# Performance work log

Hardware: AMD Instinct MI355X
Metric: run time of the kernel (lower is better)

Reference implementation:

```python
import jax, jax.numpy as jnp
import numpy as np

N = 8192; S = 32; M = 8; H = 64; DIM = 3
DELTA_T = 0.1; WELL_WIDTH = 1.0; WELL_DEPTH = 1.0
LN_EPS = 1e-5; FOUR_PI = 4.0 * np.pi


def _mlp(x, W1, b1, g, h, W2, b2):
    # eqx: Linear -> LayerNorm -> relu -> Linear, vmapped over cells
    y = x @ W1.T + b1
    mu = y.mean(-1, keepdims=True)
    var = y.var(-1, keepdims=True)
    y = g * (y - mu) / jnp.sqrt(var + LN_EPS) + h
    return jax.nn.relu(y) @ W2.T + b2


def setup_inputs():
    key = jax.random.key(0)
    ks = jax.random.split(key, 16)
    w = lambda k, shape, s=0.05: jax.random.normal(k, shape, jnp.float32) * s
    return {
        "position": jax.random.normal(ks[0], (N, DIM), jnp.float32) * 10.0,
        "radius": jax.random.uniform(ks[1], (N,), jnp.float32, 0.5, 1.5),
        "state": jax.random.uniform(ks[2], (N, S), jnp.float32),
        "diffusion_coefs": jax.random.uniform(ks[3], (M,), jnp.float32, 0.5, 2.0),
        "degradation_rates": jax.random.uniform(ks[4], (M,), jnp.float32, 0.1, 1.0),
        "Wsec1": w(ks[5], (H, S)), "bsec1": jnp.zeros((H,)), "gsec": jnp.ones((H,)), "hsec": jnp.zeros((H,)),
        "Wsec2": w(ks[6], (M, H)), "bsec2": jnp.zeros((M,)),
        "Wsen1": w(ks[7], (H, S + M)), "bsen1": jnp.zeros((H,)), "gsen": jnp.ones((H,)), "hsen": jnp.zeros((H,)),
        "Wsen2": w(ks[8], (S, H)), "bsen2": jnp.zeros((S,)),
        "Wr1": w(ks[9], (H, S)), "br1": jnp.zeros((H,)), "gr": jnp.ones((H,)), "hr": jnp.zeros((H,)),
        "Wr2": w(ks[10], (S, H)), "br2": jnp.zeros((S,)),
        "Wm1": w(ks[11], (H, S)), "bm1": jnp.zeros((H,)), "gm": jnp.ones((H,)), "hm": jnp.zeros((H,)),
        "Wm2": w(ks[12], (DIM, H)), "bm2": jnp.zeros((DIM,)),
        "active": jnp.ones((N,), bool),
    }


def _forward(position, radius, state, diffusion_coefs, degradation_rates,
             Wsec1, bsec1, gsec, hsec, Wsec2, bsec2,
             Wsen1, bsen1, gsen, hsen, Wsen2, bsen2,
             Wr1, br1, gr, hr, Wr2, br2,
             Wm1, bm1, gm, hm, Wm2, bm2,
             active):
    act = active.astype(position.dtype)
    # pairwise distances (N, N) without materializing (N, N, 3)
    sq = jnp.sum(position * position, axis=-1)
    d2 = sq[:, None] + sq[None, :] - 2.0 * (position @ position.T)
    d = jnp.sqrt(jnp.clip(d2, 1e-12))
    # --- SecretionModel: relu MLP over state ---
    secretion = jax.nn.relu(_mlp(state, Wsec1, bsec1, gsec, hsec, Wsec2, bsec2)) * act[:, None]
    # --- DiffusionModel: steady-state Green's fn exp(-r/lambda) / (4 pi D r) ---
    d_eff = jnp.maximum(d, radius[None, :])  # regularize at/inside source cell
    conc = []
    for m in range(M):  # small fixed loop over molecules
        Dm = jnp.clip(diffusion_coefs[m], 1e-3)
        km = jnp.clip(degradation_rates[m], 1e-3)
        lam = jnp.sqrt(Dm / km)
        K = jnp.exp(-d_eff / lam) / (FOUR_PI * Dm * d_eff)  # (N, N)
        conc.append(K @ secretion[:, m])
    concentration = jnp.stack(conc, axis=-1) * act[:, None]  # (N, M)
    # --- SensationModel: state += MLP([state, concentration]) ---
    state = state + _mlp(jnp.concatenate([state, concentration], axis=-1),
                         Wsen1, bsen1, gsen, hsen, Wsen2, bsen2)
    # --- ReactModel: state += sigmoid(MLP(state)) ---
    state = state + jax.nn.sigmoid(_mlp(state, Wr1, br1, gr, hr, Wr2, br2))
    # --- MotilityModel: per-cell force ---
    motility = _mlp(state, Wm1, bm1, gm, hm, Wm2, bm2)  # (N, DIM)
    # --- MechanicsModel: pairwise Morse force, F_i = sum_j f(d_ij) (p_i - p_j)/d_ij ---
    a = 1.0 / WELL_WIDTH
    re = radius[:, None] + radius[None, :]
    e = jnp.exp(-a * (d - re))
    fmag = 2.0 * a * WELL_DEPTH * (e * e - e)  # = -dU/dd, repulsive for d < re
    mask = act[:, None] * act[None, :] * (1.0 - jnp.eye(d.shape[0], dtype=d.dtype))
    coef = fmag * mask / d  # (N, N)
    mech = position * coef.sum(axis=1, keepdims=True) - coef @ position  # avoids (N,N,3)
    # --- integrate positions ---
    force = (mech + motility) * act[:, None]
    position = position + DELTA_T * force
    return jnp.concatenate([position, state, concentration], axis=-1)  # (N, DIM+S+M)


def reference(position, radius, state, diffusion_coefs, degradation_rates,
              Wsec1, bsec1, gsec, hsec, Wsec2, bsec2,
              Wsen1, bsen1, gsen, hsen, Wsen2, bsen2,
              Wr1, br1, gr, hr, Wr2, br2,
              Wm1, bm1, gm, hm, Wm2, bm2,
              active):
    return _forward(position, radius, state, diffusion_coefs, degradation_rates,
                    Wsec1, bsec1, gsec, hsec, Wsec2, bsec2,
                    Wsen1, bsen1, gsen, hsen, Wsen2, bsen2,
                    Wr1, br1, gr, hr, Wr2, br2,
                    Wm1, bm1, gm, hm, Wm2, bm2,
                    active)
```

## Files before the change

kernel.cpp:

```cpp
#include <hip/hip_runtime.h>
#include <math.h>

#define N_CELLS 8192
#define S_DIM   32
#define M_MOL   8
#define H_DIM   64
#define LN_EPS  1e-5f
#define FOUR_PI 12.566370614359172f
#define LOG2E   1.4426950408889634f
#define DT      0.1f

#define TI      4

#define REC_F    16
#define PART_OFF (N_CELLS * REC_F)
#define PART_F   12
#define WS_NEED(NJC) ((size_t)(PART_OFF + (size_t)N_CELLS * (NJC) * PART_F) * 4)

typedef float v2f __attribute__((ext_vector_type(2)));

__device__ __forceinline__ v2f vfma2(v2f a, v2f b, v2f c) {
#if __has_builtin(__builtin_elementwise_fma)
    return __builtin_elementwise_fma(a, b, c);
#else
    v2f r; r.x = fmaf(a.x, b.x, c.x); r.y = fmaf(a.y, b.y, c.y); return r;
#endif
}
__device__ __forceinline__ v2f vmax2(v2f a, v2f b) {
#if __has_builtin(__builtin_elementwise_max)
    return __builtin_elementwise_max(a, b);
#else
    v2f r; r.x = fmaxf(a.x, b.x); r.y = fmaxf(a.y, b.y); return r;
#endif
}
__device__ __forceinline__ v2f vmin2(v2f a, v2f b) {
#if __has_builtin(__builtin_elementwise_min)
    return __builtin_elementwise_min(a, b);
#else
    v2f r; r.x = fminf(a.x, b.x); r.y = fminf(a.y, b.y); return r;
#endif
}

__device__ __forceinline__ float fast_exp2(float x) {
#if __has_builtin(__builtin_amdgcn_exp2f)
    return __builtin_amdgcn_exp2f(x);
#else
    return exp2f(x);
#endif
}
__device__ __forceinline__ float fast_rcp(float x) {
#if __has_builtin(__builtin_amdgcn_rcpf)
    return __builtin_amdgcn_rcpf(x);
#else
    return 1.0f / x;
#endif
}
__device__ __forceinline__ float fast_rsqrt(float x) {
#if __has_builtin(__builtin_amdgcn_rsqf)
    return __builtin_amdgcn_rsqf(x);
#else
    return rsqrtf(x);
#endif
}
__device__ __forceinline__ float fast_log2(float x) {
#if __has_builtin(__builtin_amdgcn_logf)
    return __builtin_amdgcn_logf(x);
#else
    return log2f(x);
#endif
}

__device__ __forceinline__ float wave_sum(float v) {
#pragma unroll
    for (int off = 32; off > 0; off >>= 1) v += __shfl_xor(v, off, 64);
    return v;
}

__device__ __forceinline__ float ln_relu(float y, const float* __restrict__ g,
                                         const float* __restrict__ hh, int lane) {
    float mu  = wave_sum(y) * (1.0f / 64.0f);
    float t   = y - mu;
    float var = wave_sum(t * t) * (1.0f / 64.0f);
    float r   = fmaf(g[lane], t * fast_rsqrt(var + LN_EPS), hh[lane]);
    return fmaxf(r, 0.0f);
}

__global__ __launch_bounds__(256) void k_secretion(
    const float* __restrict__ pos, const float* __restrict__ radius,
    const float* __restrict__ state, const float* __restrict__ dc,
    const float* __restrict__ dr,
    const float* __restrict__ W1, const float* __restrict__ b1,
    const float* __restrict__ g,  const float* __restrict__ hh,
    const float* __restrict__ W2, const float* __restrict__ b2,
    float* __restrict__ ws)
{
    __shared__ float W1t[S_DIM * H_DIM];
    __shared__ float W2o[M_MOL * H_DIM];

    int tid = threadIdx.x;
    for (int idx = tid; idx < S_DIM * H_DIM; idx += 256) {
        int h = idx / S_DIM, k = idx % S_DIM;
        W1t[k * H_DIM + h] = W1[idx];
    }
    for (int idx = tid; idx < M_MOL * H_DIM; idx += 256) W2o[idx] = W2[idx];

    float* acc = ws + PART_OFF;
    int gtid = blockIdx.x * 256 + tid;
    if (gtid < N_CELLS * PART_F) acc[gtid] = 0.0f;
    __syncthreads();

    int lane = tid & 63, wid = tid >> 6;
    int wave = blockIdx.x * 4 + wid;
#pragma unroll
    for (int c = 0; c < 2; ++c) {
        int cell = wave * 2 + c;
        float x = (lane < S_DIM) ? state[cell * S_DIM + lane] : 0.0f;
        float y = b1[lane];
#pragma unroll
        for (int k = 0; k < S_DIM; ++k)
            y = fmaf(W1t[k * H_DIM + lane], __shfl(x, k, 64), y);
        float yr = ln_relu(y, g, hh, lane);

        float sp[M_MOL];
#pragma unroll
        for (int m = 0; m < M_MOL; ++m) {
            float sm = wave_sum(W2o[m * H_DIM + lane] * yr) + b2[m];
            sm = fmaxf(sm, 0.0f);
            float Dm = fmaxf(dc[m], 1e-3f);
            sp[m] = fast_log2(fmaxf(sm / (FOUR_PI * Dm), 1e-38f));
        }
        float negc_slot = 0.0f;
        if (cell < M_MOL) {
            float Dm = fmaxf(dc[cell], 1e-3f);
            float km = fmaxf(dr[cell], 1e-3f);
            negc_slot = -LOG2E * sqrtf(km / Dm);
        }
        float px = pos[cell * 3 + 0], py = pos[cell * 3 + 1], pz = pos[cell * 3 + 2];
        float r = radius[cell];
        float invr = fast_rcp(r);
        float4 v;
        if (lane == 0)      v = make_float4(px, py, pz, r);
        else if (lane == 1) v = make_float4(invr, r * LOG2E, sp[0], sp[1]);
        else if (lane == 2) v = make_float4(sp[2], sp[3], sp[4], sp[5]);
        else                v = make_float4(sp[6], sp[7], negc_slot, 0.0f);
        if (lane < 4) ((float4*)ws)[cell * 4 + lane] = v;
    }
}

#define PAIR2(PX, PY, PZ, RIL, C0A, C0B, C0C, C0D, C1A, C1B, C1C, C1D, FX, FY, FZ) \
    {                                                                        \
        v2f dx = PX - pjx, dy = PY - pjy, dz = PZ - pjz;                     \
        v2f d2 = dx * dx; d2 = vfma2(dy, dy, d2); d2 = vfma2(dz, dz, d2);    \
        v2f epsv; epsv.x = 1e-12f; epsv.y = 1e-12f;                          \
        d2 = vmax2(d2, epsv);                                                \
        v2f rsq; rsq.x = fast_rsqrt(d2.x); rsq.y = fast_rsqrt(d2.y);         \
        v2f dd = d2 * rsq;                                                   \
        v2f arg = vfma2(dd, negL2, RIL + rlg);                               \
        v2f e; e.x = fast_exp2(arg.x); e.y = fast_exp2(arg.y);               \
        v2f q = vfma2(e, e, -e);                                             \
        v2f coef = q * rsq;                                                  \
        FX = vfma2(coef, dx, FX);                                            \
        FY = vfma2(coef, dy, FY);                                            \
        FZ = vfma2(coef, dz, FZ);                                            \
        v2f de = vmax2(dd, rj2);                                             \
        v2f iv = vmin2(rsq, ivr);                                            \
        {                                                                    \
            v2f de2; de2.x = de.x; de2.y = de.x;                             \
            v2f iv2; iv2.x = iv.x; iv2.y = iv.x;                             \
            v2f a0 = vfma2(de2, ng01, ls01);                                 \
            v2f a1 = vfma2(de2, ng23, ls23);                                 \
            v2f a2 = vfma2(de2, ng45, ls45);                                 \
            v2f a3 = vfma2(de2, ng67, ls67);                                 \
            v2f e0; e0.x = fast_exp2(a0.x); e0.y = fast_exp2(a0.y);          \
            v2f e1; e1.x = fast_exp2(a1.x); e1.y = fast_exp2(a1.y);          \
            v2f e2; e2.x = fast_exp2(a2.x); e2.y = fast_exp2(a2.y);          \
            v2f e3; e3.x = fast_exp2(a3.x); e3.y = fast_exp2(a3.y);          \
            C0A = vfma2(e0, iv2, C0A);                                       \
            C0B = vfma2(e1, iv2, C0B);                                       \
            C0C = vfma2(e2, iv2, C0C);                                       \
            C0D = vfma2(e3, iv2, C0D);                                       \
        }                                                                    \
        {                                                                    \
            v2f de2; de2.x = de.y; de2.y = de.y;                             \
            v2f iv2; iv2.x = iv.y; iv2.y = iv.y;                             \
            v2f a0 = vfma2(de2, ng01, ls01);                                 \
            v2f a1 = vfma2(de2, ng23, ls23);                                 \
            v2f a2 = vfma2(de2, ng45, ls45);                                 \
            v2f a3 = vfma2(de2, ng67, ls67);                                 \
            v2f e0; e0.x = fast_exp2(a0.x); e0.y = fast_exp2(a0.y);          \
            v2f e1; e1.x = fast_exp2(a1.x); e1.y = fast_exp2(a1.y);          \
            v2f e2; e2.x = fast_exp2(a2.x); e2.y = fast_exp2(a2.y);          \
            v2f e3; e3.x = fast_exp2(a3.x); e3.y = fast_exp2(a3.y);          \
            C1A = vfma2(e0, iv2, C1A);                                       \
            C1B = vfma2(e1, iv2, C1B);                                       \
            C1C = vfma2(e2, iv2, C1C);                                       \
            C1D = vfma2(e3, iv2, C1D);                                       \
        }                                                                    \
    }

template <int JC_T>
__global__ __launch_bounds__(256, 4) void k_pairwise(
    float* __restrict__ ws, int use_part)
{
    constexpr int NJC_T = N_CELLS / JC_T;
    __shared__ float4 Ls[JC_T * 4];
    int tid = threadIdx.x;
    int jbase = blockIdx.y * JC_T;
    const float4* rec4 = (const float4*)ws;
    for (int idx = tid; idx < JC_T * 4; idx += 256)
        Ls[idx] = rec4[jbase * 4 + idx];

    v2f ng01; ng01.x = ws[0 * REC_F + 14]; ng01.y = ws[1 * REC_F + 14];
    v2f ng23; ng23.x = ws[2 * REC_F + 14]; ng23.y = ws[3 * REC_F + 14];
    v2f ng45; ng45.x = ws[4 * REC_F + 14]; ng45.y = ws[5 * REC_F + 14];
    v2f ng67; ng67.x = ws[6 * REC_F + 14]; ng67.y = ws[7 * REC_F + 14];

    v2f negL2; negL2.x = -LOG2E; negL2.y = -LOG2E;

    int i0 = blockIdx.x * (256 * TI) + tid;
    float4 me0 = rec4[(size_t)(i0      ) * 4];
    float4 me1 = rec4[(size_t)(i0 + 256) * 4];
    float4 me2 = rec4[(size_t)(i0 + 512) * 4];
    float4 me3 = rec4[(size_t)(i0 + 768) * 4];
    v2f pxA; pxA.x = me0.x; pxA.y = me1.x;
    v2f pyA; pyA.x = me0.y; pyA.y = me1.y;
    v2f pzA; pzA.x = me0.z; pzA.y = me1.z;
    v2f riA; riA.x = me0.w * LOG2E; riA.y = me1.w * LOG2E;
    v2f pxB; pxB.x = me2.x; pxB.y = me3.x;
    v2f pyB; pyB.x = me2.y; pyB.y = me3.y;
    v2f pzB; pzB.x = me2.z; pzB.y = me3.z;
    v2f riB; riB.x = me2.w * LOG2E; riB.y = me3.w * LOG2E;

    v2f r0c0 = {0,0}, r0c1 = {0,0}, r0c2 = {0,0}, r0c3 = {0,0};
    v2f r1c0 = {0,0}, r1c1 = {0,0}, r1c2 = {0,0}, r1c3 = {0,0};
    v2f r2c0 = {0,0}, r2c1 = {0,0}, r2c2 = {0,0}, r2c3 = {0,0};
    v2f r3c0 = {0,0}, r3c1 = {0,0}, r3c2 = {0,0}, r3c3 = {0,0};
    v2f fAx = {0,0}, fAy = {0,0}, fAz = {0,0};
    v2f fBx = {0,0}, fBy = {0,0}, fBz = {0,0};
    __syncthreads();

#pragma unroll 2
    for (int jj = 0; jj < JC_T; ++jj) {
        float4 A  = Ls[jj * 4 + 0];
        float4 B  = Ls[jj * 4 + 1];
        float4 Cc = Ls[jj * 4 + 2];
        float4 Dd = Ls[jj * 4 + 3];
        v2f pjx; pjx.x = A.x; pjx.y = A.x;
        v2f pjy; pjy.x = A.y; pjy.y = A.y;
        v2f pjz; pjz.x = A.z; pjz.y = A.z;
        v2f rj2; rj2.x = A.w; rj2.y = A.w;
        v2f ivr; ivr.x = B.x; ivr.y = B.x;
        v2f rlg; rlg.x = B.y; rlg.y = B.y;
        v2f ls01; ls01.x = B.z;  ls01.y = B.w;
        v2f ls23; ls23.x = Cc.x; ls23.y = Cc.y;
        v2f ls45; ls45.x = Cc.z; ls45.y = Cc.w;
        v2f ls67; ls67.x = Dd.x; ls67.y = Dd.y;
        PAIR2(pxA, pyA, pzA, riA, r0c0, r0c1, r0c2, r0c3,
              r1c0, r1c1, r1c2, r1c3, fAx, fAy, fAz)
        PAIR2(pxB, pyB, pzB, riB, r2c0, r2c1, r2c2, r2c3,
              r3c0, r3c1, r3c2, r3c3, fBx, fBy, fBz)
    }

    if (use_part) {
#define STORE_ROW(IR, CA, CB, CCX, CD, FX, FY, FZ)                               \
        {                                                                        \
            float* p = ws + PART_OFF + (size_t)((IR) * NJC_T + blockIdx.y) * PART_F; \
            ((float4*)p)[0] = make_float4(CA.x, CA.y, CB.x, CB.y);               \
            ((float4*)p)[1] = make_float4(CCX.x, CCX.y, CD.x, CD.y);             \
            ((float4*)p)[2] = make_float4((FX) + (FX), (FY) + (FY), (FZ) + (FZ), 0.0f); \
        }
        STORE_ROW(i0,       r0c0, r0c1, r0c2, r0c3, fAx.x, fAy.x, fAz.x)
        STORE_ROW(i0 + 256, r1c0, r1c1, r1c2, r1c3, fAx.y, fAy.y, fAz.y)
        STORE_ROW(i0 + 512, r2c0, r2c1, r2c2, r2c3, fBx.x, fBy.x, fBz.x)
        STORE_ROW(i0 + 768, r3c0, r3c1, r3c2, r3c3, fBx.y, fBy.y, fBz.y)
#undef STORE_ROW
    } else {
#define ATOM_ROW(IR, CA, CB, CCX, CD, FX, FY, FZ)                                \
        {                                                                        \
            float* a = ws + PART_OFF + (size_t)(IR) * PART_F;                    \
            atomicAdd(&a[0], CA.x); atomicAdd(&a[1], CA.y);                      \
            atomicAdd(&a[2], CB.x); atomicAdd(&a[3], CB.y);                      \
            atomicAdd(&a[4], CCX.x); atomicAdd(&a[5], CCX.y);                    \
            atomicAdd(&a[6], CD.x); atomicAdd(&a[7], CD.y);                      \
            atomicAdd(&a[8], (FX) + (FX)); atomicAdd(&a[9], (FY) + (FY));        \
            atomicAdd(&a[10], (FZ) + (FZ));                                      \
        }
        ATOM_ROW(i0,       r0c0, r0c1, r0c2, r0c3, fAx.x, fAy.x, fAz.x)
        ATOM_ROW(i0 + 256, r1c0, r1c1, r1c2, r1c3, fAx.y, fAy.y, fAz.y)
        ATOM_ROW(i0 + 512, r2c0, r2c1, r2c2, r2c3, fBx.x, fBy.x, fBz.x)
        ATOM_ROW(i0 + 768, r3c0, r3c1, r3c2, r3c3, fBx.y, fBy.y, fBz.y)
#undef ATOM_ROW
    }
}

__global__ __launch_bounds__(256, 4) void k_update(
    const float* __restrict__ pos,   const float* __restrict__ state,
    const float* __restrict__ Wsen1, const float* __restrict__ bsen1,
    const float* __restrict__ gsen,  const float* __restrict__ hsen,
    const float* __restrict__ Wsen2, const float* __restrict__ bsen2,
    const float* __restrict__ Wr1,   const float* __restrict__ br1,
    const float* __restrict__ gr,    const float* __restrict__ hr,
    const float* __restrict__ Wr2,   const float* __restrict__ br2,
    const float* __restrict__ Wm1,   const float* __restrict__ bm1,
    const float* __restrict__ gm,    const float* __restrict__ hm,
    const float* __restrict__ Wm2,   const float* __restrict__ bm2,
    const float* __restrict__ ws,    float* __restrict__ out,
    int use_part, int njc)
{
    __shared__ float Ws1t[40 * 64];
    __shared__ float Ws2t[64 * 32];
    __shared__ float Wr1t[32 * 64];
    __shared__ float Wr2t[64 * 32];
    __shared__ float Wm1t[32 * 64];
    __shared__ float Wm2o[3 * 64];

    int tid = threadIdx.x;
    for (int idx = tid; idx < 40 * 64; idx += 256) { int h = idx / 40, k = idx % 40; Ws1t[k * 64 + h] = Wsen1[idx]; }
    for (int idx = tid; idx < 32 * 64; idx += 256) { int o = idx / 64, h = idx % 64; Ws2t[h * 32 + o] = Wsen2[idx]; }
    for (int idx = tid; idx < 32 * 64; idx += 256) { int h = idx / 32, k = idx % 32; Wr1t[k * 64 + h] = Wr1[idx]; }
    for (int idx = tid; idx < 32 * 64; idx += 256) { int o = idx / 64, h = idx % 64; Wr2t[h * 32 + o] = Wr2[idx]; }
    for (int idx = tid; idx < 32 * 64; idx += 256) { int h = idx / 32, k = idx % 32; Wm1t[k * 64 + h] = Wm1[idx]; }
    for (int idx = tid; idx < 3 * 64;  idx += 256) Wm2o[idx] = Wm2[idx];
    __syncthreads();

    int lane = tid & 63, wid = tid >> 6;
    int wave = blockIdx.x * 4 + wid;
    int o = lane & 31;
    int idx8 = lane & 7;

#pragma unroll
    for (int c = 0; c < 2; ++c) {
        int cell = wave * 2 + c;

        float r[12];
        if (use_part) {
#pragma unroll
            for (int m = 0; m < 12; ++m) r[m] = 0.0f;
            for (int s = lane; s < njc; s += 64) {
                const float* pb = ws + PART_OFF + (size_t)(cell * njc + s) * PART_F;
                float4 v0 = ((const float4*)pb)[0];
                float4 v1 = ((const float4*)pb)[1];
                float4 v2 = ((const float4*)pb)[2];
                r[0] += v0.x; r[1] += v0.y; r[2]  += v0.z; r[3]  += v0.w;
                r[4] += v1.x; r[5] += v1.y; r[6]  += v1.z; r[7]  += v1.w;
                r[8] += v2.x; r[9] += v2.y; r[10] += v2.z;
            }
#pragma unroll
            for (int m = 0; m < 11; ++m) r[m] = wave_sum(r[m]);
        } else {
            const float* ac = ws + PART_OFF + (size_t)cell * PART_F;
#pragma unroll
            for (int m = 0; m < 11; ++m) r[m] = ac[m];
        }
        float cv = r[0];
        cv = (idx8 == 1) ? r[1] : cv;
        cv = (idx8 == 2) ? r[2] : cv;
        cv = (idx8 == 3) ? r[3] : cv;
        cv = (idx8 == 4) ? r[4] : cv;
        cv = (idx8 == 5) ? r[5] : cv;
        cv = (idx8 == 6) ? r[6] : cv;
        cv = (idx8 == 7) ? r[7] : cv;

        float s_reg = (lane < 32) ? state[cell * 32 + lane] : 0.0f;

        float x = (lane < 32) ? s_reg : ((lane < 40) ? cv : 0.0f);
        float y = bsen1[lane];
#pragma unroll
        for (int k = 0; k < 40; ++k) y = fmaf(Ws1t[k * 64 + lane], __shfl(x, k, 64), y);
        float yr = ln_relu(y, gsen, hsen, lane);
        float a2 = 0.0f;
#pragma unroll
        for (int h = 0; h < 64; ++h) a2 = fmaf(Ws2t[h * 32 + o], __shfl(yr, h, 64), a2);
        s_reg += a2 + bsen2[o];

        y = br1[lane];
#pragma unroll
        for (int k = 0; k < 32; ++k) y = fmaf(Wr1t[k * 64 + lane], __shfl(s_reg, k, 64), y);
        yr = ln_relu(y, gr, hr, lane);
        a2 = 0.0f;
#pragma unroll
        for (int h = 0; h < 64; ++h) a2 = fmaf(Wr2t[h * 32 + o], __shfl(yr, h, 64), a2);
        a2 += br2[o];
        s_reg += fast_rcp(1.0f + fast_exp2(-a2 * LOG2E));

        y = bm1[lane];
#pragma unroll
        for (int k = 0; k < 32; ++k) y = fmaf(Wm1t[k * 64 + lane], __shfl(s_reg, k, 64), y);
        yr = ln_relu(y, gm, hm, lane);
        float mot[3];
#pragma unroll
        for (int m = 0; m < 3; ++m) mot[m] = wave_sum(Wm2o[m * 64 + lane] * yr) + bm2[m];

        float px = pos[cell * 3 + 0], py = pos[cell * 3 + 1], pz = pos[cell * 3 + 2];
        float nx = fmaf(DT, r[8] + mot[0], px);
        float ny = fmaf(DT, r[9] + mot[1], py);
        float nz = fmaf(DT, r[10] + mot[2], pz);

        float* orow = out + (size_t)cell * 43;
        float pv = (lane == 0) ? nx : ((lane == 1) ? ny : nz);
        if (lane < 3)  orow[lane] = pv;
        if (lane < 32) orow[3 + lane] = s_reg;
        if (lane < 8)  orow[35 + lane] = cv;
    }
}

extern "C" void kernel_launch(void* const* d_in, const int* in_sizes, int n_in,
                              void* d_out, int out_size, void* d_ws, size_t ws_size,
                              hipStream_t stream) {
    const float* pos    = (const float*)d_in[0];
    const float* radius = (const float*)d_in[1];
    const float* state  = (const float*)d_in[2];
    const float* dc     = (const float*)d_in[3];
    const float* dr     = (const float*)d_in[4];
    const float* Wsec1  = (const float*)d_in[5];
    const float* bsec1  = (const float*)d_in[6];
    const float* gsec   = (const float*)d_in[7];
    const float* hsec   = (const float*)d_in[8];
    const float* Wsec2  = (const float*)d_in[9];
    const float* bsec2  = (const float*)d_in[10];
    const float* Wsen1  = (const float*)d_in[11];
    const float* bsen1  = (const float*)d_in[12];
    const float* gsen   = (const float*)d_in[13];
    const float* hsen   = (const float*)d_in[14];
    const float* Wsen2  = (const float*)d_in[15];
    const float* bsen2  = (const float*)d_in[16];
    const float* Wr1    = (const float*)d_in[17];
    const float* br1    = (const float*)d_in[18];
    const float* gr     = (const float*)d_in[19];
    const float* hr     = (const float*)d_in[20];
    const float* Wr2    = (const float*)d_in[21];
    const float* br2    = (const float*)d_in[22];
    const float* Wm1    = (const float*)d_in[23];
    const float* bm1    = (const float*)d_in[24];
    const float* gm     = (const float*)d_in[25];
    const float* hm     = (const float*)d_in[26];
    const float* Wm2    = (const float*)d_in[27];
    const float* bm2    = (const float*)d_in[28];
    float* ws  = (float*)d_ws;
    float* out = (float*)d_out;

    int njc, use_part;
    if (ws_size >= WS_NEED(256))      { njc = 256; use_part = 1; }
    else if (ws_size >= WS_NEED(128)) { njc = 128; use_part = 1; }
    else if (ws_size >= WS_NEED(64))  { njc = 64;  use_part = 1; }
    else                              { njc = 64;  use_part = 0; }

    hipLaunchKernelGGL(k_secretion, dim3(1024), dim3(256), 0, stream,
                       pos, radius, state, dc, dr,
                       Wsec1, bsec1, gsec, hsec, Wsec2, bsec2, ws);
    if (njc == 256) {
        hipLaunchKernelGGL((k_pairwise<32>), dim3(N_CELLS / (256 * TI), 256), dim3(256), 0,
                           stream, ws, use_part);
    } else if (njc == 128) {
        hipLaunchKernelGGL((k_pairwise<64>), dim3(N_CELLS / (256 * TI), 128), dim3(256), 0,
                           stream, ws, use_part);
    } else {
        hipLaunchKernelGGL((k_pairwise<128>), dim3(N_CELLS / (256 * TI), 64), dim3(256), 0,
                           stream, ws, use_part);
    }
    hipLaunchKernelGGL(k_update, dim3(1024), dim3(256), 0, stream,
                       pos, state,
                       Wsen1, bsen1, gsen, hsen, Wsen2, bsen2,
                       Wr1, br1, gr, hr, Wr2, br2,
                       Wm1, bm1, gm, hm, Wm2, bm2,
                       ws, out, use_part, njc);
}
```

Before: 269.8 us.

## Fuse secretion, pairwise and update stages into one cooperative kernel

Replaces the three-kernel pipeline with a single cooperative kernel of 1024 blocks that runs secretion, the pairwise pass over 128 j-chunks and the per-cell update, separated by grid-wide syncs. The goal is to remove two kernel launch gaps and the partial-buffer zeroing by having every block write its own partial slots directly. It also fixes the j-chunking at 128 instead of choosing it from workspace size. Risks are the cost of the grid syncs, the need for all 1024 blocks to be co-resident (4 per CU at 256 threads), and a fallback path that drops the partial buffers when the cooperative launch fails.

```diff
diff --git a/kernel.cpp b/kernel.cpp
--- a/kernel.cpp
+++ b/kernel.cpp
@@ -1,4 +1,5 @@
 #include <hip/hip_runtime.h>
+#include <hip/hip_cooperative_groups.h>
 #include <math.h>
 
 #define N_CELLS 8192
@@ -17,6 +18,10 @@
 #define PART_F   12
 #define WS_NEED(NJC) ((size_t)(PART_OFF + (size_t)N_CELLS * (NJC) * PART_F) * 4)
 
+#define FBLK   1024
+#define NJC_F  128
+#define JC_F   64
+
 typedef float v2f __attribute__((ext_vector_type(2)));
 
 __device__ __forceinline__ v2f vfma2(v2f a, v2f b, v2f c) {
@@ -83,68 +88,6 @@
     float var = wave_sum(t * t) * (1.0f / 64.0f);
     float r   = fmaf(g[lane], t * fast_rsqrt(var + LN_EPS), hh[lane]);
     return fmaxf(r, 0.0f);
-}
-
-__global__ __launch_bounds__(256) void k_secretion(
-    const float* __restrict__ pos, const float* __restrict__ radius,
-    const float* __restrict__ state, const float* __restrict__ dc,
-    const float* __restrict__ dr,
-    const float* __restrict__ W1, const float* __restrict__ b1,
-    const float* __restrict__ g,  const float* __restrict__ hh,
-    const float* __restrict__ W2, const float* __restrict__ b2,
-    float* __restrict__ ws)
-{
-    __shared__ float W1t[S_DIM * H_DIM];
-    __shared__ float W2o[M_MOL * H_DIM];
-
-    int tid = threadIdx.x;
-    for (int idx = tid; idx < S_DIM * H_DIM; idx += 256) {
-        int h = idx / S_DIM, k = idx % S_DIM;
-        W1t[k * H_DIM + h] = W1[idx];
-    }
-    for (int idx = tid; idx < M_MOL * H_DIM; idx += 256) W2o[idx] = W2[idx];
-
-    float* acc = ws + PART_OFF;
-    int gtid = blockIdx.x * 256 + tid;
-    if (gtid < N_CELLS * PART_F) acc[gtid] = 0.0f;
-    __syncthreads();
-
-    int lane = tid & 63, wid = tid >> 6;
-    int wave = blockIdx.x * 4 + wid;
-#pragma unroll
-    for (int c = 0; c < 2; ++c) {
-        int cell = wave * 2 + c;
-        float x = (lane < S_DIM) ? state[cell * S_DIM + lane] : 0.0f;
-        float y = b1[lane];
-#pragma unroll
-        for (int k = 0; k < S_DIM; ++k)
-            y = fmaf(W1t[k * H_DIM + lane], __shfl(x, k, 64), y);
-        float yr = ln_relu(y, g, hh, lane);
-
-        float sp[M_MOL];
-#pragma unroll
-        for (int m = 0; m < M_MOL; ++m) {
-            float sm = wave_sum(W2o[m * H_DIM + lane] * yr) + b2[m];
-            sm = fmaxf(sm, 0.0f);
-            float Dm = fmaxf(dc[m], 1e-3f);
-            sp[m] = fast_log2(fmaxf(sm / (FOUR_PI * Dm), 1e-38f));
-        }
-        float negc_slot = 0.0f;
-        if (cell < M_MOL) {
-            float Dm = fmaxf(dc[cell], 1e-3f);
-            float km = fmaxf(dr[cell], 1e-3f);
-            negc_slot = -LOG2E * sqrtf(km / Dm);
-        }
-        float px = pos[cell * 3 + 0], py = pos[cell * 3 + 1], pz = pos[cell * 3 + 2];
-        float r = radius[cell];
-        float invr = fast_rcp(r);
-        float4 v;
-        if (lane == 0)      v = make_float4(px, py, pz, r);
-        else if (lane == 1) v = make_float4(invr, r * LOG2E, sp[0], sp[1]);
-        else if (lane == 2) v = make_float4(sp[2], sp[3], sp[4], sp[5]);
-        else                v = make_float4(sp[6], sp[7], negc_slot, 0.0f);
-        if (lane < 4) ((float4*)ws)[cell * 4 + lane] = v;
-    }
 }
 
 #define PAIR2(PX, PY, PZ, RIL, C0A, C0B, C0C, C0D, C1A, C1B, C1C, C1D, FX, FY, FZ) \
@@ -198,6 +141,331 @@
         }                                                                    \
     }
 
+struct Params {
+    const float* pos; const float* radius; const float* state;
+    const float* dc;  const float* dr;
+    const float* Wsec1; const float* bsec1; const float* gsec; const float* hsec;
+    const float* Wsec2; const float* bsec2;
+    const float* Wsen1; const float* bsen1; const float* gsen; const float* hsen;
+    const float* Wsen2; const float* bsen2;
+    const float* Wr1; const float* br1; const float* gr; const float* hr;
+    const float* Wr2; const float* br2;
+    const float* Wm1; const float* bm1; const float* gm; const float* hm;
+    const float* Wm2; const float* bm2;
+    float* ws; float* out;
+};
+
+__global__ __launch_bounds__(256, 4) void k_fused(Params P)
+{
+    __shared__ float4 Ls[JC_F * 4];
+    __shared__ float  shBig[4608];
+
+    cooperative_groups::grid_group grid = cooperative_groups::this_grid();
+
+    int tid  = threadIdx.x;
+    int bid  = blockIdx.x;
+    int lane = tid & 63, wid = tid >> 6;
+
+    {
+        float* W1t = shBig;
+        float* W2o = shBig + 2048;
+        for (int idx = tid; idx < S_DIM * H_DIM; idx += 256) {
+            int h = idx / S_DIM, k = idx % S_DIM;
+            W1t[k * H_DIM + h] = P.Wsec1[idx];
+        }
+        for (int idx = tid; idx < M_MOL * H_DIM; idx += 256) W2o[idx] = P.Wsec2[idx];
+        __syncthreads();
+
+#pragma unroll
+        for (int c = 0; c < 2; ++c) {
+            int cell = bid * 8 + wid * 2 + c;
+            float x = (lane < S_DIM) ? P.state[cell * S_DIM + lane] : 0.0f;
+            float y = P.bsec1[lane];
+#pragma unroll
+            for (int k = 0; k < S_DIM; ++k)
+                y = fmaf(W1t[k * H_DIM + lane], __shfl(x, k, 64), y);
+            float yr = ln_relu(y, P.gsec, P.hsec, lane);
+
+            float sp[M_MOL];
+#pragma unroll
+            for (int m = 0; m < M_MOL; ++m) {
+                float sm = wave_sum(W2o[m * H_DIM + lane] * yr) + P.bsec2[m];
+                sm = fmaxf(sm, 0.0f);
+                float Dm = fmaxf(P.dc[m], 1e-3f);
+                sp[m] = fast_log2(fmaxf(sm / (FOUR_PI * Dm), 1e-38f));
+            }
+            float negc_slot = 0.0f;
+            if (cell < M_MOL) {
+                float Dm = fmaxf(P.dc[cell], 1e-3f);
+                float km = fmaxf(P.dr[cell], 1e-3f);
+                negc_slot = -LOG2E * sqrtf(km / Dm);
+            }
+            float px = P.pos[cell * 3 + 0], py = P.pos[cell * 3 + 1], pz = P.pos[cell * 3 + 2];
+            float r = P.radius[cell];
+            float invr = fast_rcp(r);
+            float4 v;
+            if (lane == 0)      v = make_float4(px, py, pz, r);
+            else if (lane == 1) v = make_float4(invr, r * LOG2E, sp[0], sp[1]);
+            else if (lane == 2) v = make_float4(sp[2], sp[3], sp[4], sp[5]);
+            else                v = make_float4(sp[6], sp[7], negc_slot, 0.0f);
+            if (lane < 4) ((float4*)P.ws)[cell * 4 + lane] = v;
+        }
+    }
+    __threadfence();
+    grid.sync();
+
+    {
+        float* ws = P.ws;
+        int bx = bid & 7;
+        int by = bid >> 3;
+        int jbase = by * JC_F;
+        const float4* rec4 = (const float4*)ws;
+        for (int idx = tid; idx < JC_F * 4; idx += 256)
+            Ls[idx] = rec4[jbase * 4 + idx];
+
+        v2f ng01; ng01.x = ws[0 * REC_F + 14]; ng01.y = ws[1 * REC_F + 14];
+        v2f ng23; ng23.x = ws[2 * REC_F + 14]; ng23.y = ws[3 * REC_F + 14];
+        v2f ng45; ng45.x = ws[4 * REC_F + 14]; ng45.y = ws[5 * REC_F + 14];
+        v2f ng67; ng67.x = ws[6 * REC_F + 14]; ng67.y = ws[7 * REC_F + 14];
+
+        v2f negL2; negL2.x = -LOG2E; negL2.y = -LOG2E;
+
+        int i0 = bx * (256 * TI) + tid;
+        float4 me0 = rec4[(size_t)(i0      ) * 4];
+        float4 me1 = rec4[(size_t)(i0 + 256) * 4];
+        float4 me2 = rec4[(size_t)(i0 + 512) * 4];
+        float4 me3 = rec4[(size_t)(i0 + 768) * 4];
+        v2f pxA; pxA.x = me0.x; pxA.y = me1.x;
+        v2f pyA; pyA.x = me0.y; pyA.y = me1.y;
+        v2f pzA; pzA.x = me0.z; pzA.y = me1.z;
+        v2f riA; riA.x = me0.w * LOG2E; riA.y = me1.w * LOG2E;
+        v2f pxB; pxB.x = me2.x; pxB.y = me3.x;
+        v2f pyB; pyB.x = me2.y; pyB.y = me3.y;
+        v2f pzB; pzB.x = me2.z; pzB.y = me3.z;
+        v2f riB; riB.x = me2.w * LOG2E; riB.y = me3.w * LOG2E;
+
+        v2f r0c0 = {0,0}, r0c1 = {0,0}, r0c2 = {0,0}, r0c3 = {0,0};
+        v2f r1c0 = {0,0}, r1c1 = {0,0}, r1c2 = {0,0}, r1c3 = {0,0};
+        v2f r2c0 = {0,0}, r2c1 = {0,0}, r2c2 = {0,0}, r2c3 = {0,0};
+        v2f r3c0 = {0,0}, r3c1 = {0,0}, r3c2 = {0,0}, r3c3 = {0,0};
+        v2f fAx = {0,0}, fAy = {0,0}, fAz = {0,0};
+        v2f fBx = {0,0}, fBy = {0,0}, fBz = {0,0};
+        __syncthreads();
+
+#pragma unroll 2
+        for (int jj = 0; jj < JC_F; ++jj) {
+            float4 A  = Ls[jj * 4 + 0];
+            float4 B  = Ls[jj * 4 + 1];
+            float4 Cc = Ls[jj * 4 + 2];
+            float4 Dd = Ls[jj * 4 + 3];
+            v2f pjx; pjx.x = A.x; pjx.y = A.x;
+            v2f pjy; pjy.x = A.y; pjy.y = A.y;
+            v2f pjz; pjz.x = A.z; pjz.y = A.z;
+            v2f rj2; rj2.x = A.w; rj2.y = A.w;
+            v2f ivr; ivr.x = B.x; ivr.y = B.x;
+            v2f rlg; rlg.x = B.y; rlg.y = B.y;
+            v2f ls01; ls01.x = B.z;  ls01.y = B.w;
+            v2f ls23; ls23.x = Cc.x; ls23.y = Cc.y;
+            v2f ls45; ls45.x = Cc.z; ls45.y = Cc.w;
+            v2f ls67; ls67.x = Dd.x; ls67.y = Dd.y;
+            PAIR2(pxA, pyA, pzA, riA, r0c0, r0c1, r0c2, r0c3,
+                  r1c0, r1c1, r1c2, r1c3, fAx, fAy, fAz)
+            PAIR2(pxB, pyB, pzB, riB, r2c0, r2c1, r2c2, r2c3,
+                  r3c0, r3c1, r3c2, r3c3, fBx, fBy, fBz)
+        }
+
+#define STORE_ROW(IR, CA, CB, CCX, CD, FX, FY, FZ)                               \
+        {                                                                        \
+            float* p = ws + PART_OFF + (size_t)((IR) * NJC_F + by) * PART_F;     \
+            ((float4*)p)[0] = make_float4(CA.x, CA.y, CB.x, CB.y);               \
+            ((float4*)p)[1] = make_float4(CCX.x, CCX.y, CD.x, CD.y);             \
+            ((float4*)p)[2] = make_float4((FX) + (FX), (FY) + (FY), (FZ) + (FZ), 0.0f); \
+        }
+        STORE_ROW(i0,       r0c0, r0c1, r0c2, r0c3, fAx.x, fAy.x, fAz.x)
+        STORE_ROW(i0 + 256, r1c0, r1c1, r1c2, r1c3, fAx.y, fAy.y, fAz.y)
+        STORE_ROW(i0 + 512, r2c0, r2c1, r2c2, r2c3, fBx.x, fBy.x, fBz.x)
+        STORE_ROW(i0 + 768, r3c0, r3c1, r3c2, r3c3, fBx.y, fBy.y, fBz.y)
+#undef STORE_ROW
+    }
+    __threadfence();
+    grid.sync();
+
+    {
+        const float* ws = P.ws;
+        int o = lane & 31;
+        int idx8 = lane & 7;
+
+        float rr[2][12];
+#pragma unroll
+        for (int c = 0; c < 2; ++c) {
+            int cell = bid * 8 + wid * 2 + c;
+#pragma unroll
+            for (int m = 0; m < 12; ++m) rr[c][m] = 0.0f;
+#pragma unroll
+            for (int s = 0; s < 2; ++s) {
+                const float* pb = ws + PART_OFF +
+                    (size_t)(cell * NJC_F + (lane + 64 * s)) * PART_F;
+                float4 v0 = ((const float4*)pb)[0];
+                float4 v1 = ((const float4*)pb)[1];
+                float4 v2 = ((const float4*)pb)[2];
+                rr[c][0] += v0.x; rr[c][1] += v0.y; rr[c][2]  += v0.z; rr[c][3] += v0.w;
+                rr[c][4] += v1.x; rr[c][5] += v1.y; rr[c][6]  += v1.z; rr[c][7] += v1.w;
+                rr[c][8] += v2.x; rr[c][9] += v2.y; rr[c][10] += v2.z;
+            }
+#pragma unroll
+            for (int m = 0; m < 11; ++m) rr[c][m] = wave_sum(rr[c][m]);
+        }
+
+        float cv[2], s_reg[2];
+#pragma unroll
+        for (int c = 0; c < 2; ++c) {
+            int cell = bid * 8 + wid * 2 + c;
+            float v = rr[c][0];
+            v = (idx8 == 1) ? rr[c][1] : v;
+            v = (idx8 == 2) ? rr[c][2] : v;
+            v = (idx8 == 3) ? rr[c][3] : v;
+            v = (idx8 == 4) ? rr[c][4] : v;
+            v = (idx8 == 5) ? rr[c][5] : v;
+            v = (idx8 == 6) ? rr[c][6] : v;
+            v = (idx8 == 7) ? rr[c][7] : v;
+            cv[c] = v;
+            s_reg[c] = (lane < 32) ? P.state[cell * 32 + lane] : 0.0f;
+        }
+
+        {
+            float* Ws1t = shBig;
+            float* Ws2t = shBig + 2560;
+            for (int idx = tid; idx < 40 * 64; idx += 256) { int h = idx / 40, k = idx % 40; Ws1t[k * 64 + h] = P.Wsen1[idx]; }
+            for (int idx = tid; idx < 32 * 64; idx += 256) { int oo = idx / 64, h = idx % 64; Ws2t[h * 32 + oo] = P.Wsen2[idx]; }
+            __syncthreads();
+#pragma unroll
+            for (int c = 0; c < 2; ++c) {
+                float x = (lane < 32) ? s_reg[c] : ((lane < 40) ? cv[c] : 0.0f);
+                float y = P.bsen1[lane];
+#pragma unroll
+                for (int k = 0; k < 40; ++k) y = fmaf(Ws1t[k * 64 + lane], __shfl(x, k, 64), y);
+                float yr = ln_relu(y, P.gsen, P.hsen, lane);
+                float a2 = 0.0f;
+#pragma unroll
+                for (int h = 0; h < 64; ++h) a2 = fmaf(Ws2t[h * 32 + o], __shfl(yr, h, 64), a2);
+                s_reg[c] += a2 + P.bsen2[o];
+            }
+            __syncthreads();
+        }
+        {
+            float* Wr1t = shBig;
+            float* Wr2t = shBig + 2048;
+            for (int idx = tid; idx < 32 * 64; idx += 256) { int h = idx / 32, k = idx % 32; Wr1t[k * 64 + h] = P.Wr1[idx]; }
+            for (int idx = tid; idx < 32 * 64; idx += 256) { int oo = idx / 64, h = idx % 64; Wr2t[h * 32 + oo] = P.Wr2[idx]; }
+            __syncthreads();
+#pragma unroll
+            for (int c = 0; c < 2; ++c) {
+                float y = P.br1[lane];
+#pragma unroll
+                for (int k = 0; k < 32; ++k) y = fmaf(Wr1t[k * 64 + lane], __shfl(s_reg[c], k, 64), y);
+                float yr = ln_relu(y, P.gr, P.hr, lane);
+                float a2 = 0.0f;
+#pragma unroll
+                for (int h = 0; h < 64; ++h) a2 = fmaf(Wr2t[h * 32 + o], __shfl(yr, h, 64), a2);
+                a2 += P.br2[o];
+                s_reg[c] += fast_rcp(1.0f + fast_exp2(-a2 * LOG2E));
+            }
+            __syncthreads();
+        }
+        {
+            float* Wm1t = shBig;
+            float* Wm2o = shBig + 2048;
+            for (int idx = tid; idx < 32 * 64; idx += 256) { int h = idx / 32, k = idx % 32; Wm1t[k * 64 + h] = P.Wm1[idx]; }
+            for (int idx = tid; idx < 3 * 64;  idx += 256) Wm2o[idx] = P.Wm2[idx];
+            __syncthreads();
+#pragma unroll
+            for (int c = 0; c < 2; ++c) {
+                int cell = bid * 8 + wid * 2 + c;
+                float y = P.bm1[lane];
+#pragma unroll
+                for (int k = 0; k < 32; ++k) y = fmaf(Wm1t[k * 64 + lane], __shfl(s_reg[c], k, 64), y);
+                float yr = ln_relu(y, P.gm, P.hm, lane);
+                float mot[3];
+#pragma unroll
+                for (int m = 0; m < 3; ++m) mot[m] = wave_sum(Wm2o[m * 64 + lane] * yr) + P.bm2[m];
+
+                float px = P.pos[cell * 3 + 0], py = P.pos[cell * 3 + 1], pz = P.pos[cell * 3 + 2];
+                float nx = fmaf(DT, rr[c][8]  + mot[0], px);
+                float ny = fmaf(DT, rr[c][9]  + mot[1], py);
+                float nz = fmaf(DT, rr[c][10] + mot[2], pz);
+
+                float* orow = P.out + (size_t)cell * 43;
+                float pv = (lane == 0) ? nx : ((lane == 1) ? ny : nz);
+                if (lane < 3)  orow[lane] = pv;
+                if (lane < 32) orow[3 + lane] = s_reg[c];
+                if (lane < 8)  orow[35 + lane] = cv[c];
+            }
+        }
+    }
+}
+
+__global__ __launch_bounds__(256) void k_secretion(
+    const float* __restrict__ pos, const float* __restrict__ radius,
+    const float* __restrict__ state, const float* __restrict__ dc,
+    const float* __restrict__ dr,
+    const float* __restrict__ W1, const float* __restrict__ b1,
+    const float* __restrict__ g,  const float* __restrict__ hh,
+    const float* __restrict__ W2, const float* __restrict__ b2,
+    float* __restrict__ ws)
+{
+    __shared__ float W1t[S_DIM * H_DIM];
+    __shared__ float W2o[M_MOL * H_DIM];
+
+    int tid = threadIdx.x;
+    for (int idx = tid; idx < S_DIM * H_DIM; idx += 256) {
+        int h = idx / S_DIM, k = idx % S_DIM;
+        W1t[k * H_DIM + h] = W1[idx];
+    }
+    for (int idx = tid; idx < M_MOL * H_DIM; idx += 256) W2o[idx] = W2[idx];
+
+    float* acc = ws + PART_OFF;
+    int gtid = blockIdx.x * 256 + tid;
+    if (gtid < N_CELLS * PART_F) acc[gtid] = 0.0f;
+    __syncthreads();
+
+    int lane = tid & 63, wid = tid >> 6;
+    int wave = blockIdx.x * 4 + wid;
+#pragma unroll
+    for (int c = 0; c < 2; ++c) {
+        int cell = wave * 2 + c;
+        float x = (lane < S_DIM) ? state[cell * S_DIM + lane] : 0.0f;
+        float y = b1[lane];
+#pragma unroll
+        for (int k = 0; k < S_DIM; ++k)
+            y = fmaf(W1t[k * H_DIM + lane], __shfl(x, k, 64), y);
+        float yr = ln_relu(y, g, hh, lane);
+
+        float sp[M_MOL];
+#pragma unroll
+        for (int m = 0; m < M_MOL; ++m) {
+            float sm = wave_sum(W2o[m * H_DIM + lane] * yr) + b2[m];
+            sm = fmaxf(sm, 0.0f);
+            float Dm = fmaxf(dc[m], 1e-3f);
+            sp[m] = fast_log2(fmaxf(sm / (FOUR_PI * Dm), 1e-38f));
+        }
+        float negc_slot = 0.0f;
+        if (cell < M_MOL) {
+            float Dm = fmaxf(dc[cell], 1e-3f);
+            float km = fmaxf(dr[cell], 1e-3f);
+            negc_slot = -LOG2E * sqrtf(km / Dm);
+        }
+        float px = pos[cell * 3 + 0], py = pos[cell * 3 + 1], pz = pos[cell * 3 + 2];
+        float r = radius[cell];
+        float invr = fast_rcp(r);
+        float4 v;
+        if (lane == 0)      v = make_float4(px, py, pz, r);
+        else if (lane == 1) v = make_float4(invr, r * LOG2E, sp[0], sp[1]);
+        else if (lane == 2) v = make_float4(sp[2], sp[3], sp[4], sp[5]);
+        else                v = make_float4(sp[6], sp[7], negc_slot, 0.0f);
+        if (lane < 4) ((float4*)ws)[cell * 4 + lane] = v;
+    }
+}
+
 template <int JC_T>
 __global__ __launch_bounds__(256, 4) void k_pairwise(
     float* __restrict__ ws, int use_part)
@@ -407,61 +675,57 @@
 extern "C" void kernel_launch(void* const* d_in, const int* in_sizes, int n_in,
                               void* d_out, int out_size, void* d_ws, size_t ws_size,
                               hipStream_t stream) {
-    const float* pos    = (const float*)d_in[0];
-    const float* radius = (const float*)d_in[1];
-    const float* state  = (const float*)d_in[2];
-    const float* dc     = (const float*)d_in[3];
-    const float* dr     = (const float*)d_in[4];
-    const float* Wsec1  = (const float*)d_in[5];
-    const float* bsec1  = (const float*)d_in[6];
-    const float* gsec   = (const float*)d_in[7];
-    const float* hsec   = (const float*)d_in[8];
-    const float* Wsec2  = (const float*)d_in[9];
-    const float* bsec2  = (const float*)d_in[10];
-    const float* Wsen1  = (const float*)d_in[11];
-    const float* bsen1  = (const float*)d_in[12];
-    const float* gsen   = (const float*)d_in[13];
-    const float* hsen   = (const float*)d_in[14];
-    const float* Wsen2  = (const float*)d_in[15];
-    const float* bsen2  = (const float*)d_in[16];
-    const float* Wr1    = (const float*)d_in[17];
-    const float* br1    = (const float*)d_in[18];
-    const float* gr     = (const float*)d_in[19];
-    const float* hr     = (const float*)d_in[20];
-    const float* Wr2    = (const float*)d_in[21];
-    const float* br2    = (const float*)d_in[22];
-    const float* Wm1    = (const float*)d_in[23];
-    const float* bm1    = (const float*)d_in[24];
-    const float* gm     = (const float*)d_in[25];
-    const float* hm     = (const float*)d_in[26];
-    const float* Wm2    = (const float*)d_in[27];
-    const float* bm2    = (const float*)d_in[28];
-    float* ws  = (float*)d_ws;
-    float* out = (float*)d_out;
-
-    int njc, use_part;
-    if (ws_size >= WS_NEED(256))      { njc = 256; use_part = 1; }
-    else if (ws_size >= WS_NEED(128)) { njc = 128; use_part = 1; }
-    else if (ws_size >= WS_NEED(64))  { njc = 64;  use_part = 1; }
-    else                              { njc = 64;  use_part = 0; }
-
-    hipLaunchKernelGGL(k_secretion, dim3(1024), dim3(256), 0, stream,
-                       pos, radius, state, dc, dr,
-                       Wsec1, bsec1, gsec, hsec, Wsec2, bsec2, ws);
-    if (njc == 256) {
-        hipLaunchKernelGGL((k_pairwise<32>), dim3(N_CELLS / (256 * TI), 256), dim3(256), 0,
-                           stream, ws, use_part);
-    } else if (njc == 128) {
-        hipLaunchKernelGGL((k_pairwise<64>), dim3(N_CELLS / (256 * TI), 128), dim3(256), 0,
-                           stream, ws, use_part);
-    } else {
-        hipLaunchKernelGGL((k_pairwise<128>), dim3(N_CELLS / (256 * TI), 64), dim3(256), 0,
-                           stream, ws, use_part);
-    }
-    hipLaunchKernelGGL(k_update, dim3(1024), dim3(256), 0, stream,
-                       pos, state,
-                       Wsen1, bsen1, gsen, hsen, Wsen2, bsen2,
-                       Wr1, br1, gr, hr, Wr2, br2,
-                       Wm1, bm1, gm, hm, Wm2, bm2,
-                       ws, out, use_part, njc);
-}
+    Params P;
+    P.pos    = (const float*)d_in[0];
+    P.radius = (const float*)d_in[1];
+    P.state  = (const float*)d_in[2];
+    P.dc     = (const float*)d_in[3];
+    P.dr     = (const float*)d_in[4];
+    P.Wsec1  = (const float*)d_in[5];
+    P.bsec1  = (const float*)d_in[6];
+    P.gsec   = (const float*)d_in[7];
+    P.hsec   = (const float*)d_in[8];
+    P.Wsec2  = (const float*)d_in[9];
+    P.bsec2  = (const float*)d_in[10];
+    P.Wsen1  = (const float*)d_in[11];
+    P.bsen1  = (const float*)d_in[12];
+    P.gsen   = (const float*)d_in[13];
+    P.hsen   = (const float*)d_in[14];
+    P.Wsen2  = (const float*)d_in[15];
+    P.bsen2  = (const float*)d_in[16];
+    P.Wr1    = (const float*)d_in[17];
+    P.br1    = (const float*)d_in[18];
+    P.gr     = (const float*)d_in[19];
+    P.hr     = (const float*)d_in[20];
+    P.Wr2    = (const float*)d_in[21];
+    P.br2    = (const float*)d_in[22];
+    P.Wm1    = (const float*)d_in[23];
+    P.bm1    = (const float*)d_in[24];
+    P.gm     = (const float*)d_in[25];
+    P.hm     = (const float*)d_in[26];
+    P.Wm2    = (const float*)d_in[27];
+    P.bm2    = (const float*)d_in[28];
+    P.ws  = (float*)d_ws;
+    P.out = (float*)d_out;
+
+    hipError_t cerr = hipErrorUnknown;
+    if (ws_size >= WS_NEED(NJC_F)) {
+        void* args[1] = { &P };
+        cerr = hipLaunchCooperativeKernel((const void*)k_fused,
+                                          dim3(FBLK), dim3(256), args, 0, stream);
+    }
+    if (cerr != hipSuccess) {
+        hipLaunchKernelGGL(k_secretion, dim3(1024), dim3(256), 0, stream,
+                           P.pos, P.radius, P.state, P.dc, P.dr,
+                           P.Wsec1, P.bsec1, P.gsec, P.hsec, P.Wsec2, P.bsec2,
+                           P.ws);
+        hipLaunchKernelGGL((k_pairwise<128>), dim3(N_CELLS / (256 * TI), 64),
+                           dim3(256), 0, stream, P.ws, 0);
+        hipLaunchKernelGGL(k_update, dim3(1024), dim3(256), 0, stream,
+                           P.pos, P.state,
+                           P.Wsen1, P.bsen1, P.gsen, P.hsen, P.Wsen2, P.bsen2,
+                           P.Wr1, P.br1, P.gr, P.hr, P.Wr2, P.br2,
+                           P.Wm1, P.bm1, P.gm, P.hm, P.Wm2, P.bm2,
+                           P.ws, P.out, 0, 64);
+    }
+}
```

Measured after the change: 755.9 us. +180.2%, slower.
